# Kernel optimization log

Hardware: AMD Instinct MI355X
Metric: run time of the kernel (lower is better)

Reference implementation:

```python
import jax, jax.numpy as jnp
import numpy as np

B, F, U, A, H = 8192, 1024, 256, 16, 8  # batch, in_features, units_layer, num_actions, hidden(=8)


def _coagent_layer(x, W0, b0, W1, b1, W2, b2):
    # x: [B, f_in]; stacked weights for U independent tiny MLPs (grouped GEMMs)
    h = jax.nn.relu(jnp.einsum('bf,uhf->buh', x, W0) + b0)   # [B, U, H]
    h = jax.nn.relu(jnp.einsum('buh,ugh->bug', h, W1) + b1)  # [B, U, H]
    q = jnp.einsum('bug,uag->bua', h, W2) + b2               # [B, U, A]
    # greedy action per coagent (epsilon-greedy with greedy=True / epsilon=0)
    return jnp.argmax(q, axis=-1).astype(jnp.float32)        # [B, U]


def setup_inputs() -> dict:
    key = jax.random.key(0)
    ks = jax.random.split(key, 19)
    n = lambda k, shape, fan: (jax.random.normal(k, shape, dtype=jnp.float32)
                               / jnp.sqrt(jnp.float32(fan)))
    return {
        'state': jax.random.normal(ks[0], (B, F), dtype=jnp.float32),
        # coagent layer 0: in_features -> 8 -> 8 -> A, stacked over U units
        'W0_0': n(ks[1], (U, H, F), F), 'b0_0': jnp.zeros((U, H), jnp.float32),
        'W1_0': n(ks[2], (U, H, H), H), 'b1_0': jnp.zeros((U, H), jnp.float32),
        'W2_0': n(ks[3], (U, A, H), H), 'b2_0': jnp.zeros((U, A), jnp.float32),
        # coagent layer 1: units_layer -> 8 -> 8 -> A, stacked over U units
        'W0_1': n(ks[4], (U, H, U), U), 'b0_1': jnp.zeros((U, H), jnp.float32),
        'W1_1': n(ks[5], (U, H, H), H), 'b1_1': jnp.zeros((U, H), jnp.float32),
        'W2_1': n(ks[6], (U, A, H), H), 'b2_1': jnp.zeros((U, A), jnp.float32),
        # Policy head: units_layer -> 8 -> 8 -> 1
        'PW0': n(ks[7], (H, U), U), 'Pb0': jnp.zeros((H,), jnp.float32),
        'PW1': n(ks[8], (H, H), H), 'Pb1': jnp.zeros((H,), jnp.float32),
        'PW2': n(ks[9], (1, H), H), 'Pb2': jnp.zeros((1,), jnp.float32),
    }


def reference(state, W0_0, b0_0, W1_0, b1_0, W2_0, b2_0,
              W0_1, b0_1, W1_1, b1_1, W2_1, b2_1,
              PW0, Pb0, PW1, Pb1, PW2, Pb2):
    a0 = _coagent_layer(state, W0_0, b0_0, W1_0, b1_0, W2_0, b2_0)  # [B, U]
    a1 = _coagent_layer(a0, W0_1, b0_1, W1_1, b1_1, W2_1, b2_1)     # [B, U]
    h = jax.nn.relu(a1 @ PW0.T + Pb0)
    h = jax.nn.relu(h @ PW1.T + Pb1)
    return h @ PW2.T + Pb2  # [B, 1]
```

## Files before the change

### kernel.cpp

```cpp
#include <hip/hip_runtime.h>
#include <cstring>
#include <cstdint>

#define B_TOTAL 8192
#define F_IN    1024
#define U_UNITS 256
#define NACT    16
#define HID     8

typedef float    f32x4  __attribute__((ext_vector_type(4)));
typedef _Float16 half8  __attribute__((ext_vector_type(8)));


__device__ __forceinline__ void gload_lds16(const _Float16* g, _Float16* l)
{
    __builtin_amdgcn_global_load_lds(
        (const __attribute__((address_space(1))) void*)g,
        (__attribute__((address_space(3))) void*)l,
        16, 0, 0);
}

__global__ __launch_bounds__(256)
void pack3_kernel(const float* __restrict__ s0, _Float16* __restrict__ d0h, _Float16* __restrict__ d0l,
                  const float* __restrict__ s1, _Float16* __restrict__ d1h, _Float16* __restrict__ d1l,
                  const float* __restrict__ s2, _Float16* __restrict__ d2h, _Float16* __restrict__ d2l)
{
    constexpr int NB0 = (B_TOTAL / 16) * (F_IN / 128);
    constexpr int NB1 = (U_UNITS * HID / 16) * (F_IN / 128);
    __shared__ float ls[16 * 132];
    int b = blockIdx.x;
    const float* src; _Float16 *dh, *dl; int K, lg;
    if (b < NB0)            { src = s0; dh = d0h; dl = d0l; K = F_IN;    lg = 3; }
    else if (b < NB0 + NB1) { b -= NB0; src = s1; dh = d1h; dl = d1l; K = F_IN; lg = 3; }
    else                    { b -= NB0 + NB1; src = s2; dh = d2h; dl = d2l; K = U_UNITS; lg = 1; }

    const int tid = threadIdx.x;
    const int mt  = b >> lg;
    const int kb  = b & ((1 << lg) - 1);
    const int r0  = mt * 16;

#pragma unroll
    for (int i = 0; i < 2; ++i) {
        const int e = tid + (i << 8);
        const int row = e >> 5;
        const int c4  = e & 31;
        f32x4 v = *reinterpret_cast<const f32x4*>(
            &src[(size_t)(r0 + row) * K + (kb << 7) + (c4 << 2)]);
        *reinterpret_cast<f32x4*>(&ls[row * 132 + (c4 << 2)]) = v;
    }
    __syncthreads();

    const int k8 = tid >> 4, r = tid & 15;
    float x[8];
#pragma unroll
    for (int j = 0; j < 8; ++j) x[j] = ls[r * 132 + (k8 << 3) + j];
    half8 h, l;
#pragma unroll
    for (int j = 0; j < 8; ++j) {
        h[j] = (_Float16)x[j];
        l[j] = (_Float16)((x[j] - (float)h[j]) * 2048.0f);
    }
    const size_t off = (((size_t)mt * (K >> 5)) + (kb << 2) + (k8 >> 2)) * 512
                     + (size_t)(((k8 & 3) << 4) + r) * 8;
    *reinterpret_cast<half8*>(&dh[off]) = h;
    *reinterpret_cast<half8*>(&dl[off]) = l;
}

constexpr int BM = 128, BN = 128;

template<int K_TOTAL, bool A_SPLIT, bool OUT_TF32>
__global__ __launch_bounds__(512, 4)
void coagent_mfma(const _Float16* __restrict__ Ahg, const _Float16* __restrict__ Alg,
                  const _Float16* __restrict__ Bhg, const _Float16* __restrict__ Blg,
                  const float* __restrict__ b0, const float* __restrict__ W1,
                  const float* __restrict__ b1, const float* __restrict__ W2,
                  const float* __restrict__ b2, void* __restrict__ outp)
{
    constexpr int BUFH  = A_SPLIT ? 16384 : 12288;
    constexpr int BOFFH = A_SPLIT ? 8192 : 4096;
    constexpr int BOFFL = A_SPLIT ? 12288 : 8192;
    constexpr int NCH   = A_SPLIT ? 4 : 3;

    struct EpiBufs { float Hs[BM][65]; _Float16 ab[BM * 8]; };
    union SMemU { _Float16 stage[2][BUFH]; EpiBufs epi; };
    __shared__ SMemU sm;

    constexpr int NTK = K_TOTAL >> 5;
    constexpr size_t TS = (size_t)NTK * 512;

    const int tid  = threadIdx.x;
    const int wave = tid >> 6;
    const int lane = tid & 63;
    const int quad = lane >> 4;
    const int l15  = lane & 15;

    const int m0 = blockIdx.y * BM;
    const int n0 = blockIdx.x * BN;

    const int wmi = wave >> 2;
    const int wni = wave & 3;
    const int at  = wmi * 4;
    const int bt  = wni * 2;
    const int wm  = wmi * 64;

    const int wave_u = __builtin_amdgcn_readfirstlane(wave);
    const _Float16* gs[NCH];
#pragma unroll
    for (int i = 0; i < NCH; ++i) {
        const int c = wave_u * NCH + i;
        const _Float16* base; int tile;
        if (A_SPLIT) {
            if (c < 8)       { base = Ahg; tile = (m0 >> 4) + c; }
            else if (c < 16) { base = Alg; tile = (m0 >> 4) + (c - 8); }
            else if (c < 24) { base = Bhg; tile = (n0 >> 4) + (c - 16); }
            else             { base = Blg; tile = (n0 >> 4) + (c - 24); }
        } else {
            if (c < 8)       { base = Ahg; tile = (m0 >> 4) + c; }
            else if (c < 16) { base = Bhg; tile = (n0 >> 4) + (c - 8); }
            else             { base = Blg; tile = (n0 >> 4) + (c - 16); }
        }
        gs[i] = base + (size_t)tile * TS;
    }
    const int loff = lane * 8;

    f32x4 acc1[4][2];
    f32x4 acc2[4][2];
#pragma unroll
    for (int i = 0; i < 4; ++i)
#pragma unroll
        for (int jj = 0; jj < 2; ++jj) { acc1[i][jj] = {0.f,0.f,0.f,0.f}; acc2[i][jj] = {0.f,0.f,0.f,0.f}; }

#pragma unroll
    for (int i = 0; i < NCH; ++i)
        gload_lds16(gs[i] + loff, &sm.stage[0][(wave_u * NCH + i) * 512]);
    __syncthreads();

    int cur = 0;
#pragma unroll 1
    for (int kt = 0; kt < NTK; ++kt) {
        if (kt + 1 < NTK) {
            _Float16* nb = &sm.stage[cur ^ 1][0];
#pragma unroll
            for (int i = 0; i < NCH; ++i)
                gload_lds16(gs[i] + (size_t)(kt + 1) * 512 + loff,
                            nb + (wave_u * NCH + i) * 512);
        }

        const _Float16* sb = &sm.stage[cur][0];
        half8 bf[2], lb[2];
#pragma unroll
        for (int nt = 0; nt < 2; ++nt) {
            bf[nt] = *reinterpret_cast<const half8*>(&sb[BOFFH + (bt + nt) * 512 + lane * 8]);
            lb[nt] = *reinterpret_cast<const half8*>(&sb[BOFFL + (bt + nt) * 512 + lane * 8]);
        }
#pragma unroll
        for (int mt = 0; mt < 4; ++mt) {
            half8 af = *reinterpret_cast<const half8*>(&sb[(at + mt) * 512 + lane * 8]);
#pragma unroll
            for (int nt = 0; nt < 2; ++nt)
                acc1[mt][nt] = __builtin_amdgcn_mfma_f32_16x16x32_f16(af, bf[nt], acc1[mt][nt], 0, 0, 0);
            if constexpr (A_SPLIT) {
                half8 la = *reinterpret_cast<const half8*>(&sb[4096 + (at + mt) * 512 + lane * 8]);
#pragma unroll
                for (int nt = 0; nt < 2; ++nt)
                    acc2[mt][nt] = __builtin_amdgcn_mfma_f32_16x16x32_f16(la, bf[nt], acc2[mt][nt], 0, 0, 0);
            }
#pragma unroll
            for (int nt = 0; nt < 2; ++nt)
                acc2[mt][nt] = __builtin_amdgcn_mfma_f32_16x16x32_f16(af, lb[nt], acc2[mt][nt], 0, 0, 0);
        }

        __syncthreads();
        cur ^= 1;
    }

    const int ubase = n0 >> 3;
    for (int half = 0; half < 2; ++half) {
        __syncthreads();
        if ((wni >> 1) == half) {
#pragma unroll
            for (int mt = 0; mt < 4; ++mt)
#pragma unroll
                for (int nt = 0; nt < 2; ++nt)
#pragma unroll
                    for (int r = 0; r < 4; ++r)
                        sm.epi.Hs[wm + mt * 16 + quad * 4 + r][(wni & 1) * 32 + nt * 16 + l15] =
                            acc1[mt][nt][r] + acc2[mt][nt][r] * (1.0f / 2048.0f);
        }
        __syncthreads();
#pragma unroll
        for (int p = 0; p < 2; ++p) {
            const int idx = (p << 9) + tid;
            const int ul = idx >> 7;
            const int bl = idx & 127;
            const int u  = __builtin_amdgcn_readfirstlane(ubase + half * 8 + ul);
            const float* __restrict__ b0u = b0 + u * 8;
            const float* __restrict__ W1u = W1 + u * 64;
            const float* __restrict__ b1u = b1 + u * 8;
            const float* __restrict__ W2u = W2 + u * 128;
            const float* __restrict__ b2u = b2 + u * 16;

            float h[HID];
#pragma unroll
            for (int jj = 0; jj < HID; ++jj)
                h[jj] = fmaxf(sm.epi.Hs[bl][ul * 8 + jj] + b0u[jj], 0.f);

            float h2[HID];
#pragma unroll
            for (int g = 0; g < HID; ++g) {
                float s = b1u[g];
#pragma unroll
                for (int jj = 0; jj < HID; ++jj)
                    s += h[jj] * W1u[g * 8 + jj];
                h2[g] = fmaxf(s, 0.f);
            }

            float best = b2u[0];
#pragma unroll
            for (int jj = 0; jj < HID; ++jj) best += h2[jj] * W2u[jj];
            int bi = 0;
#pragma unroll
            for (int a = 1; a < NACT; ++a) {
                float s = b2u[a];
#pragma unroll
                for (int jj = 0; jj < HID; ++jj)
                    s += h2[jj] * W2u[a * 8 + jj];
                if (s > best) { best = s; bi = a; }
            }

            if (OUT_TF32) {
                ((float*)outp)[(size_t)u * B_TOTAL + m0 + bl] = (float)bi;
            } else {
                sm.epi.ab[bl * 8 + ul] = (_Float16)bi;
            }
        }
        if (!OUT_TF32) {
            __syncthreads();
            if (tid < 128) {
                float4 v = *reinterpret_cast<float4*>(&sm.epi.ab[tid * 8]);
                const int u = ubase + half * 8;
                const int b = m0 + tid;
                const size_t off = ((size_t)(b >> 4) * 8 + (u >> 5)) * 512
                                 + (size_t)((((u >> 3) & 3) << 4) + (b & 15)) * 8;
                *reinterpret_cast<float4*>(&((_Float16*)outp)[off]) = v;
            }
        }
    }
}


constexpr int FBM = 128, FBN = 128, FBK = 16;

template<int K_TOTAL, bool X_TRANSPOSED>
__global__ __launch_bounds__(256, 2)
void coagent_kernel(const float* __restrict__ X, const float* __restrict__ W0,
                    const float* __restrict__ b0, const float* __restrict__ W1,
                    const float* __restrict__ b1, const float* __restrict__ W2,
                    const float* __restrict__ b2, float* __restrict__ outT)
{
    struct SMemGemm { float As[FBK][FBM + 4]; float Bs[FBK][FBN + 4]; };
    union SMem { SMemGemm g; float Hs[FBM][65]; };
    __shared__ SMem sm;

    const int tid = threadIdx.x;
    const int tx = tid & 15, ty = tid >> 4;
    const int m0 = blockIdx.y * FBM, n0 = blockIdx.x * FBN;

    float acc[8][8];
#pragma unroll
    for (int i = 0; i < 8; ++i)
#pragma unroll
        for (int j = 0; j < 8; ++j) acc[i][j] = 0.f;

    for (int k0 = 0; k0 < K_TOTAL; k0 += FBK) {
        __syncthreads();
        if (X_TRANSPOSED) {
#pragma unroll
            for (int l = tid; l < (FBM * FBK) / 4; l += 256) {
                const int k = l >> 5, q = l & 31;
                const float4 v = *reinterpret_cast<const float4*>(
                    &X[(size_t)(k0 + k) * B_TOTAL + m0 + 4 * q]);
                *reinterpret_cast<float4*>(&sm.g.As[k][4 * q]) = v;
            }
        } else {
#pragma unroll
            for (int l = tid; l < (FBM * FBK) / 4; l += 256) {
                const int row = l >> 2, c = l & 3;
                const float4 v = *reinterpret_cast<const float4*>(
                    &X[(size_t)(m0 + row) * K_TOTAL + k0 + 4 * c]);
                sm.g.As[4 * c + 0][row] = v.x; sm.g.As[4 * c + 1][row] = v.y;
                sm.g.As[4 * c + 2][row] = v.z; sm.g.As[4 * c + 3][row] = v.w;
            }
        }
#pragma unroll
        for (int l = tid; l < (FBN * FBK) / 4; l += 256) {
            const int row = l >> 2, c = l & 3;
            const float4 v = *reinterpret_cast<const float4*>(
                &W0[(size_t)(n0 + row) * K_TOTAL + k0 + 4 * c]);
            sm.g.Bs[4 * c + 0][row] = v.x; sm.g.Bs[4 * c + 1][row] = v.y;
            sm.g.Bs[4 * c + 2][row] = v.z; sm.g.Bs[4 * c + 3][row] = v.w;
        }
        __syncthreads();
#pragma unroll
        for (int k = 0; k < FBK; ++k) {
            float a[8], bb[8];
            *reinterpret_cast<float4*>(&a[0])  = *reinterpret_cast<float4*>(&sm.g.As[k][4 * ty]);
            *reinterpret_cast<float4*>(&a[4])  = *reinterpret_cast<float4*>(&sm.g.As[k][64 + 4 * ty]);
            *reinterpret_cast<float4*>(&bb[0]) = *reinterpret_cast<float4*>(&sm.g.Bs[k][4 * tx]);
            *reinterpret_cast<float4*>(&bb[4]) = *reinterpret_cast<float4*>(&sm.g.Bs[k][64 + 4 * tx]);
#pragma unroll
            for (int i = 0; i < 8; ++i)
#pragma unroll
                for (int j = 0; j < 8; ++j) acc[i][j] += a[i] * bb[j];
        }
    }

    const int ub_base = n0 >> 3;
    for (int half = 0; half < 2; ++half) {
        __syncthreads();
#pragma unroll
        for (int i = 0; i < 8; ++i) {
            const int row = (i < 4) ? (4 * ty + i) : (64 + 4 * ty + (i - 4));
#pragma unroll
            for (int j = 0; j < 4; ++j)
                sm.Hs[row][4 * tx + j] = acc[i][4 * half + j];
        }
        __syncthreads();
#pragma unroll
        for (int p = 0; p < 4; ++p) {
            const int pair = (p << 8) + tid;
            const int ul = pair >> 7, bl = pair & 127;
            const int u = ub_base + half * 8 + ul;
            float h[HID];
#pragma unroll
            for (int j = 0; j < HID; ++j)
                h[j] = fmaxf(sm.Hs[bl][ul * 8 + j] + b0[u * 8 + j], 0.f);
            float h2[HID];
#pragma unroll
            for (int g = 0; g < HID; ++g) {
                float s = b1[u * 8 + g];
#pragma unroll
                for (int j = 0; j < HID; ++j) s += h[j] * W1[u * 64 + g * 8 + j];
                h2[g] = fmaxf(s, 0.f);
            }
            float best = b2[u * 16];
#pragma unroll
            for (int j = 0; j < HID; ++j) best += h2[j] * W2[u * 128 + j];
            int bi = 0;
#pragma unroll
            for (int a = 1; a < NACT; ++a) {
                float s = b2[u * 16 + a];
#pragma unroll
                for (int j = 0; j < HID; ++j) s += h2[j] * W2[u * 128 + a * 8 + j];
                if (s > best) { best = s; bi = a; }
            }
            outT[(size_t)u * B_TOTAL + m0 + bl] = (float)bi;
        }
    }
}

__global__ __launch_bounds__(256)
void policy_kernel(const float* __restrict__ A1T,
                   const float* __restrict__ PW0, const float* __restrict__ Pb0,
                   const float* __restrict__ PW1, const float* __restrict__ Pb1,
                   const float* __restrict__ PW2, const float* __restrict__ Pb2,
                   float* __restrict__ out)
{
    __shared__ float part[8][32][HID + 1];
    const int tid = threadIdx.x;
    const int b32 = tid & 31;
    const int sl  = tid >> 5;
    const int b   = blockIdx.x * 32 + b32;

    float hp[HID];
#pragma unroll
    for (int j = 0; j < HID; ++j) hp[j] = 0.f;

#pragma unroll 1
    for (int q0 = 0; q0 < 32; q0 += 8) {
        float v[8];
#pragma unroll
        for (int t = 0; t < 8; ++t)
            v[t] = A1T[(size_t)(sl * 32 + q0 + t) * B_TOTAL + b];
#pragma unroll
        for (int t = 0; t < 8; ++t)
#pragma unroll
            for (int j = 0; j < HID; ++j)
                hp[j] += v[t] * PW0[j * U_UNITS + sl * 32 + q0 + t];
    }
#pragma unroll
    for (int j = 0; j < HID; ++j) part[sl][b32][j] = hp[j];
    __syncthreads();

    if (sl == 0) {
        float h[HID];
#pragma unroll
        for (int j = 0; j < HID; ++j) {
            float s = Pb0[j];
#pragma unroll
            for (int s8 = 0; s8 < 8; ++s8) s += part[s8][b32][j];
            h[j] = fmaxf(s, 0.f);
        }
        float h2[HID];
#pragma unroll
        for (int g = 0; g < HID; ++g) {
            float s = Pb1[g];
#pragma unroll
            for (int j = 0; j < HID; ++j) s += h[j] * PW1[g * 8 + j];
            h2[g] = fmaxf(s, 0.f);
        }
        float o = Pb2[0];
#pragma unroll
        for (int j = 0; j < HID; ++j) o += h2[j] * PW2[j];
        out[b] = o;
    }
}


extern "C" void kernel_launch(void* const* d_in, const int* in_sizes, int n_in,
                              void* d_out, int out_size, void* d_ws, size_t ws_size,
                              hipStream_t stream)
{
    const float* state = (const float*)d_in[0];
    const float* W0_0  = (const float*)d_in[1];
    const float* b0_0  = (const float*)d_in[2];
    const float* W1_0  = (const float*)d_in[3];
    const float* b1_0  = (const float*)d_in[4];
    const float* W2_0  = (const float*)d_in[5];
    const float* b2_0  = (const float*)d_in[6];
    const float* W0_1  = (const float*)d_in[7];
    const float* b0_1  = (const float*)d_in[8];
    const float* W1_1  = (const float*)d_in[9];
    const float* b1_1  = (const float*)d_in[10];
    const float* W2_1  = (const float*)d_in[11];
    const float* b2_1  = (const float*)d_in[12];
    const float* PW0   = (const float*)d_in[13];
    const float* Pb0   = (const float*)d_in[14];
    const float* PW1   = (const float*)d_in[15];
    const float* Pb1   = (const float*)d_in[16];
    const float* PW2   = (const float*)d_in[17];
    const float* Pb2   = (const float*)d_in[18];

    const size_t SZ_STATE = (size_t)B_TOTAL * F_IN;
    const size_t SZ_W00   = (size_t)U_UNITS * HID * F_IN;
    const size_t SZ_W01   = (size_t)U_UNITS * HID * U_UNITS;
    const size_t NEED = (2 * SZ_STATE + 2 * SZ_W00 + 2 * SZ_W01
                         + (size_t)B_TOTAL * U_UNITS) * 2
                        + (size_t)U_UNITS * B_TOTAL * 4;

    if (ws_size >= NEED) {
        char* p = (char*)d_ws;
        _Float16* state_h = (_Float16*)p;                p += SZ_STATE * 2;
        _Float16* state_l = (_Float16*)p;                p += SZ_STATE * 2;
        _Float16* w00_h   = (_Float16*)p;                p += SZ_W00 * 2;
        _Float16* w00_l   = (_Float16*)p;                p += SZ_W00 * 2;
        _Float16* w01_h   = (_Float16*)p;                p += SZ_W01 * 2;
        _Float16* w01_l   = (_Float16*)p;                p += SZ_W01 * 2;
        _Float16* a0      = (_Float16*)p;                p += (size_t)B_TOTAL * U_UNITS * 2;
        float*    a1T     = (float*)p;

        constexpr int NB0 = (B_TOTAL / 16) * (F_IN / 128);
        constexpr int NB1 = (U_UNITS * HID / 16) * (F_IN / 128);
        constexpr int NB2 = (U_UNITS * HID / 16) * (U_UNITS / 128);
        pack3_kernel<<<NB0 + NB1 + NB2, 256, 0, stream>>>(
            state, state_h, state_l, W0_0, w00_h, w00_l, W0_1, w01_h, w01_l);

        dim3 grid((U_UNITS * HID) / BN, B_TOTAL / BM);

        coagent_mfma<F_IN, true, false><<<grid, 512, 0, stream>>>(
            state_h, state_l, w00_h, w00_l, b0_0, W1_0, b1_0, W2_0, b2_0, (void*)a0);

        coagent_mfma<U_UNITS, false, true><<<grid, 512, 0, stream>>>(
            a0, nullptr, w01_h, w01_l, b0_1, W1_1, b1_1, W2_1, b2_1, (void*)a1T);

        policy_kernel<<<B_TOTAL / 32, 256, 0, stream>>>(
            a1T, PW0, Pb0, PW1, Pb1, PW2, Pb2, (float*)d_out);
    } else {
        float* a0T = (float*)d_ws;
        float* a1T = a0T + (size_t)U_UNITS * B_TOTAL;
        dim3 grid((U_UNITS * HID) / FBN, B_TOTAL / FBM);
        coagent_kernel<F_IN, false><<<grid, 256, 0, stream>>>(
            state, W0_0, b0_0, W1_0, b1_0, W2_0, b2_0, a0T);
        coagent_kernel<U_UNITS, true><<<grid, 256, 0, stream>>>(
            a0T, W0_1, b0_1, W1_1, b1_1, W2_1, b2_1, a1T);
        policy_kernel<<<B_TOTAL / 32, 256, 0, stream>>>(
            a1T, PW0, Pb0, PW1, Pb1, PW2, Pb2, (float*)d_out);
    }
}
```

Measured before the change: 267.6 us.

## Triple-buffer LDS staging with one barrier per step for split-A GEMM

For the split-precision (A_SPLIT) instantiation, the K loop moves from double to triple LDS buffering. Loads are issued two tiles ahead, and completion is tracked with explicit vmcnt waits plus a single raw barrier per iteration, replacing the two syncthreads per step. The intent is to hide global-to-LDS latency and cut barrier stalls. In exchange, LDS use grows by half and launch bounds drop to 2 blocks per CU, which lowers occupancy and relies on the hand-written vmcnt counts being correct.

```diff
diff --git a/kernel.cpp b/kernel.cpp
--- a/kernel.cpp
+++ b/kernel.cpp
@@ -69,7 +69,7 @@
 constexpr int BM = 128, BN = 128;
 
 template<int K_TOTAL, bool A_SPLIT, bool OUT_TF32>
-__global__ __launch_bounds__(512, 4)
+__global__ __launch_bounds__(512, A_SPLIT ? 2 : 4)
 void coagent_mfma(const _Float16* __restrict__ Ahg, const _Float16* __restrict__ Alg,
                   const _Float16* __restrict__ Bhg, const _Float16* __restrict__ Blg,
                   const float* __restrict__ b0, const float* __restrict__ W1,
@@ -80,9 +80,10 @@
     constexpr int BOFFH = A_SPLIT ? 8192 : 4096;
     constexpr int BOFFL = A_SPLIT ? 12288 : 8192;
     constexpr int NCH   = A_SPLIT ? 4 : 3;
+    constexpr int NBUF  = A_SPLIT ? 3 : 2;
 
     struct EpiBufs { float Hs[BM][65]; _Float16 ab[BM * 8]; };
-    union SMemU { _Float16 stage[2][BUFH]; EpiBufs epi; };
+    union SMemU { _Float16 stage[NBUF][BUFH]; EpiBufs epi; };
     __shared__ SMemU sm;
 
     constexpr int NTK = K_TOTAL >> 5;
@@ -130,48 +131,97 @@
 #pragma unroll
         for (int jj = 0; jj < 2; ++jj) { acc1[i][jj] = {0.f,0.f,0.f,0.f}; acc2[i][jj] = {0.f,0.f,0.f,0.f}; }
 
-#pragma unroll
-    for (int i = 0; i < NCH; ++i)
-        gload_lds16(gs[i] + loff, &sm.stage[0][(wave_u * NCH + i) * 512]);
-    __syncthreads();
-
-    int cur = 0;
+    if constexpr (A_SPLIT) {
+        _Float16* bA = &sm.stage[0][0];
+        _Float16* bB = &sm.stage[1][0];
+        _Float16* bC = &sm.stage[2][0];
+
+#pragma unroll
+        for (int i = 0; i < NCH; ++i)
+            gload_lds16(gs[i] + loff, bA + (wave_u * NCH + i) * 512);
+#pragma unroll
+        for (int i = 0; i < NCH; ++i)
+            gload_lds16(gs[i] + 512 + loff, bB + (wave_u * NCH + i) * 512);
+
 #pragma unroll 1
-    for (int kt = 0; kt < NTK; ++kt) {
-        if (kt + 1 < NTK) {
-            _Float16* nb = &sm.stage[cur ^ 1][0];
-#pragma unroll
-            for (int i = 0; i < NCH; ++i)
-                gload_lds16(gs[i] + (size_t)(kt + 1) * 512 + loff,
-                            nb + (wave_u * NCH + i) * 512);
-        }
-
-        const _Float16* sb = &sm.stage[cur][0];
-        half8 bf[2], lb[2];
-#pragma unroll
-        for (int nt = 0; nt < 2; ++nt) {
-            bf[nt] = *reinterpret_cast<const half8*>(&sb[BOFFH + (bt + nt) * 512 + lane * 8]);
-            lb[nt] = *reinterpret_cast<const half8*>(&sb[BOFFL + (bt + nt) * 512 + lane * 8]);
-        }
-#pragma unroll
-        for (int mt = 0; mt < 4; ++mt) {
-            half8 af = *reinterpret_cast<const half8*>(&sb[(at + mt) * 512 + lane * 8]);
-#pragma unroll
-            for (int nt = 0; nt < 2; ++nt)
-                acc1[mt][nt] = __builtin_amdgcn_mfma_f32_16x16x32_f16(af, bf[nt], acc1[mt][nt], 0, 0, 0);
-            if constexpr (A_SPLIT) {
-                half8 la = *reinterpret_cast<const half8*>(&sb[4096 + (at + mt) * 512 + lane * 8]);
+        for (int kt = 0; kt < NTK; ++kt) {
+            if (kt + 1 < NTK) asm volatile("s_waitcnt vmcnt(4)" ::: "memory");
+            else              asm volatile("s_waitcnt vmcnt(0)" ::: "memory");
+            __builtin_amdgcn_s_barrier();
+            __builtin_amdgcn_sched_barrier(0);
+
+            if (kt + 2 < NTK) {
+#pragma unroll
+                for (int i = 0; i < NCH; ++i)
+                    gload_lds16(gs[i] + (size_t)(kt + 2) * 512 + loff,
+                                bC + (wave_u * NCH + i) * 512);
+            }
+
+            const _Float16* sb = bA;
+            half8 bf[2], lb[2];
+#pragma unroll
+            for (int nt = 0; nt < 2; ++nt) {
+                bf[nt] = *reinterpret_cast<const half8*>(&sb[BOFFH + (bt + nt) * 512 + lane * 8]);
+                lb[nt] = *reinterpret_cast<const half8*>(&sb[BOFFL + (bt + nt) * 512 + lane * 8]);
+            }
+#pragma unroll
+            for (int mt = 0; mt < 4; ++mt) {
+                half8 af = *reinterpret_cast<const half8*>(&sb[(at + mt) * 512 + lane * 8]);
 #pragma unroll
                 for (int nt = 0; nt < 2; ++nt)
-                    acc2[mt][nt] = __builtin_amdgcn_mfma_f32_16x16x32_f16(la, bf[nt], acc2[mt][nt], 0, 0, 0);
-            }
-#pragma unroll
-            for (int nt = 0; nt < 2; ++nt)
-                acc2[mt][nt] = __builtin_amdgcn_mfma_f32_16x16x32_f16(af, lb[nt], acc2[mt][nt], 0, 0, 0);
-        }
-
-        __syncthreads();
-        cur ^= 1;
+                    acc1[mt][nt] = __builtin_amdgcn_mfma_f32_16x16x32_f16(af, bf[nt], acc1[mt][nt], 0, 0, 0);
+                {
+                    half8 la = *reinterpret_cast<const half8*>(&sb[4096 + (at + mt) * 512 + lane * 8]);
+#pragma unroll
+                    for (int nt = 0; nt < 2; ++nt)
+                        acc2[mt][nt] = __builtin_amdgcn_mfma_f32_16x16x32_f16(la, bf[nt], acc2[mt][nt], 0, 0, 0);
+                }
+#pragma unroll
+                for (int nt = 0; nt < 2; ++nt)
+                    acc2[mt][nt] = __builtin_amdgcn_mfma_f32_16x16x32_f16(af, lb[nt], acc2[mt][nt], 0, 0, 0);
+            }
+
+            _Float16* t = bA; bA = bB; bB = bC; bC = t;
+        }
+        __syncthreads();
+    } else {
+#pragma unroll
+        for (int i = 0; i < NCH; ++i)
+            gload_lds16(gs[i] + loff, &sm.stage[0][(wave_u * NCH + i) * 512]);
+        __syncthreads();
+
+        int cur = 0;
+#pragma unroll 1
+        for (int kt = 0; kt < NTK; ++kt) {
+            if (kt + 1 < NTK) {
+                _Float16* nb = &sm.stage[cur ^ 1][0];
+#pragma unroll
+                for (int i = 0; i < NCH; ++i)
+                    gload_lds16(gs[i] + (size_t)(kt + 1) * 512 + loff,
+                                nb + (wave_u * NCH + i) * 512);
+            }
+
+            const _Float16* sb = &sm.stage[cur][0];
+            half8 bf[2], lb[2];
+#pragma unroll
+            for (int nt = 0; nt < 2; ++nt) {
+                bf[nt] = *reinterpret_cast<const half8*>(&sb[BOFFH + (bt + nt) * 512 + lane * 8]);
+                lb[nt] = *reinterpret_cast<const half8*>(&sb[BOFFL + (bt + nt) * 512 + lane * 8]);
+            }
+#pragma unroll
+            for (int mt = 0; mt < 4; ++mt) {
+                half8 af = *reinterpret_cast<const half8*>(&sb[(at + mt) * 512 + lane * 8]);
+#pragma unroll
+                for (int nt = 0; nt < 2; ++nt)
+                    acc1[mt][nt] = __builtin_amdgcn_mfma_f32_16x16x32_f16(af, bf[nt], acc1[mt][nt], 0, 0, 0);
+#pragma unroll
+                for (int nt = 0; nt < 2; ++nt)
+                    acc2[mt][nt] = __builtin_amdgcn_mfma_f32_16x16x32_f16(af, lb[nt], acc2[mt][nt], 0, 0, 0);
+            }
+
+            __syncthreads();
+            cur ^= 1;
+        }
     }
 
     const int ubase = n0 >> 3;
```

Result: slower. 300.1 us (+12.1%).
